# Optimization experiments

Hardware: AMD Instinct MI355X
Metric: run time of the kernel (lower is better)

## Reference

```python
import jax, jax.numpy as jnp
import numpy as np

N_NODES = 100000
N_EDGES = 3200000
IN_F = 256
OUT_F = 128


def setup_inputs() -> dict:
    key = jax.random.key(0)
    k1, k2, k3, k4, k5, k6 = jax.random.split(key, 6)
    x = jax.random.normal(k1, (N_NODES, IN_F), dtype=jnp.float32)
    edge_row = jax.random.randint(k2, (N_EDGES,), 0, N_NODES, dtype=jnp.int32)
    edge_col = jax.random.randint(k3, (N_EDGES,), 0, N_NODES, dtype=jnp.int32)
    edge_val = jax.random.uniform(k4, (N_EDGES,), dtype=jnp.float32)
    stdv = 1.0 / np.sqrt(OUT_F)
    weight = jax.random.uniform(k5, (IN_F, OUT_F), dtype=jnp.float32, minval=-stdv, maxval=stdv)
    bias = jax.random.uniform(k6, (OUT_F,), dtype=jnp.float32, minval=-stdv, maxval=stdv)
    return {"x": x, "edge_row": edge_row, "edge_col": edge_col,
            "edge_val": edge_val, "weight": weight, "bias": bias}


def reference(x, edge_row, edge_col, edge_val, weight, bias):
    # dropout p=0.0 -> identity. support = x @ W  [N, out_f]
    support = x @ weight
    # spmm(adj, support): out[r] = sum_e adj_val[e] * support[col[e]] for edges with row[e]==r
    gathered = support[edge_col] * edge_val[:, None]  # [E, out_f]
    out = jax.ops.segment_sum(gathered, edge_row, num_segments=N_NODES)
    out = out + bias
    return jax.nn.relu(out)
```

## Files before the change

kernel.cpp:

```cpp
#include <hip/hip_runtime.h>
#include <hip/hip_fp16.h>

#define IN_F 256
#define OUT_F 128
#define RPB 64
#define LOG_RPB 6
#define MAXB 2048
#define CHUNK 8192
#define CAP 3072

typedef __attribute__((ext_vector_type(8))) short short8;
typedef __attribute__((ext_vector_type(4))) float f32x4;

__device__ inline short bf16r(float f) {
  unsigned u = __float_as_uint(f);
  u += 0x7FFF + ((u >> 16) & 1);
  return (short)(u >> 16);
}

#define COL_OF(e) ((e) & 0x1FFFFu)
#define Q9_OF(e)  (((e) >> 17) & 0x1FFu)
#define RL_OF(e)  ((e) >> 26)

__global__ __launch_bounds__(256) void hist_wprep(const int* __restrict__ erow,
                                                  int* __restrict__ cnt2d,
                                                  const float* __restrict__ w,
                                                  short* __restrict__ wt,
                                                  int n_edges, int nbuck, int nblk) {
  __shared__ int h[MAXB];
  int t = threadIdx.x;
  if ((int)blockIdx.x >= nblk) {
    int i = (blockIdx.x - nblk) * 1024 + t * 4;
#pragma unroll
    for (int u = 0; u < 4; ++u) {
      int idx = i + u;
      int k = idx >> 7;
      int n = idx & 127;
      wt[n * 256 + k] = bf16r(w[idx]);
    }
    return;
  }
  for (int i = t; i < nbuck; i += 256) h[i] = 0;
  __syncthreads();
  int beg = blockIdx.x * CHUNK;
  int end = min(beg + CHUNK, n_edges);
  for (int e = beg + t; e < end; e += 256) atomicAdd(&h[erow[e] >> LOG_RPB], 1);
  __syncthreads();
  for (int i = t; i < nbuck; i += 256) cnt2d[(size_t)i * nblk + blockIdx.x] = h[i];
}

__global__ __launch_bounds__(256) void rowsum(const int* __restrict__ cnt2d,
                                              int* __restrict__ bcnt, int nblk) {
  __shared__ int red[256];
  int b = blockIdx.x;
  const int* row = cnt2d + (size_t)b * nblk;
  int t = threadIdx.x;
  int s = 0;
  for (int i = t; i < nblk; i += 256) s += row[i];
  red[t] = s;
  __syncthreads();
  for (int off = 128; off > 0; off >>= 1) {
    if (t < off) red[t] += red[t + off];
    __syncthreads();
  }
  if (t == 0) bcnt[b] = red[0];
}

__global__ __launch_bounds__(1024) void bucket_scan(const int* __restrict__ bcnt,
                                                    int* __restrict__ bptr, int nbuck) {
  __shared__ int sc[1024];
  int t = threadIdx.x;
  int i0 = 2 * t, i1 = 2 * t + 1;
  int c0 = (i0 < nbuck) ? bcnt[i0] : 0;
  int c1 = (i1 < nbuck) ? bcnt[i1] : 0;
  int s = c0 + c1;
  sc[t] = s;
  __syncthreads();
  for (int off = 1; off < 1024; off <<= 1) {
    int u = (t >= off) ? sc[t - off] : 0;
    __syncthreads();
    sc[t] += u;
    __syncthreads();
  }
  int run = sc[t] - s;
  if (i0 < nbuck) { bptr[i0] = run; run += c0; }
  if (i1 < nbuck) { bptr[i1] = run; run += c1; }
  if (t == 1023) bptr[nbuck] = sc[1023];
}

__global__ __launch_bounds__(256) void rowscan(const int* __restrict__ cnt2d,
                                               const int* __restrict__ bptr,
                                               int* __restrict__ off2d, int nblk) {
  __shared__ int sc[256];
  int b = blockIdx.x;
  const int* row = cnt2d + (size_t)b * nblk;
  int* orow = off2d + (size_t)b * nblk;
  int t = threadIdx.x;
  int chunk = (nblk + 255) >> 8;
  int beg = t * chunk, end2 = min(beg + chunk, nblk);
  int s = 0;
  for (int i = beg; i < end2; ++i) s += row[i];
  sc[t] = s;
  __syncthreads();
  for (int off = 1; off < 256; off <<= 1) {
    int u = (t >= off) ? sc[t - off] : 0;
    __syncthreads();
    sc[t] += u;
    __syncthreads();
  }
  int run = sc[t] - s + bptr[b];
  for (int i = beg; i < end2; ++i) {
    orow[i] = run;
    run += row[i];
  }
}

__global__ __launch_bounds__(512) void gemm_coarse(const float* __restrict__ x,
                                                   const short* __restrict__ wt,
                                                   __half* __restrict__ sup,
                                                   int n_nodes,
                                                   const int* __restrict__ erow,
                                                   const int* __restrict__ ecol,
                                                   const float* __restrict__ eval,
                                                   const int* __restrict__ off2d,
                                                   unsigned* __restrict__ tmp,
                                                   int n_edges, int nbuck, int nblk,
                                                   int ngemm) {
  __shared__ int cnt[MAXB];
  __shared__ int base[MAXB];
  int t = threadIdx.x;

  if ((int)blockIdx.x >= ngemm) {
    int cb = blockIdx.x - ngemm;
    for (int i = t; i < nbuck; i += 512) {
      cnt[i] = 0;
      base[i] = off2d[(size_t)i * nblk + cb];
    }
    __syncthreads();
    int beg = cb * CHUNK;
    int end = min(beg + CHUNK, n_edges);
    for (int e = beg + t; e < end; e += 512) {
      int r = erow[e];
      int b = r >> LOG_RPB;
      int pos = base[b] + atomicAdd(&cnt[b], 1);
      float v = eval[e];
      int q = min(max((int)(v * 511.f + 0.5f), 0), 511);
      tmp[pos] = (unsigned)ecol[e] | ((unsigned)q << 17) |
                 ((unsigned)(r & (RPB - 1)) << 26);
    }
    return;
  }

  int lane = t & 63;
  int wid = t >> 6;
  int wrow = (wid >> 1) * 32;
  int wcol = (wid & 1) * 64;
  int row_blk = blockIdx.x * 128;

  int arow[2];
#pragma unroll
  for (int mt = 0; mt < 2; ++mt)
    arow[mt] = min(row_blk + wrow + mt * 16 + (lane & 15), n_nodes - 1);
  int koff = (lane >> 4) * 8;

  f32x4 acc[2][4];
#pragma unroll
  for (int mt = 0; mt < 2; ++mt)
#pragma unroll
    for (int nt = 0; nt < 4; ++nt) acc[mt][nt] = (f32x4){0.f, 0.f, 0.f, 0.f};

#pragma unroll 2
  for (int kk = 0; kk < IN_F; kk += 32) {
    short8 af[2];
#pragma unroll
    for (int mt = 0; mt < 2; ++mt) {
      const float* px = x + (size_t)arow[mt] * IN_F + kk + koff;
      float4 p = *(const float4*)px;
      float4 q = *(const float4*)(px + 4);
      short8 a;
      a[0] = bf16r(p.x); a[1] = bf16r(p.y); a[2] = bf16r(p.z); a[3] = bf16r(p.w);
      a[4] = bf16r(q.x); a[5] = bf16r(q.y); a[6] = bf16r(q.z); a[7] = bf16r(q.w);
      af[mt] = a;
    }
    short8 bf[4];
#pragma unroll
    for (int nt = 0; nt < 4; ++nt) {
      int n = wcol + nt * 16 + (lane & 15);
      bf[nt] = *(const short8*)&wt[n * 256 + kk + koff];
    }
#pragma unroll
    for (int mt = 0; mt < 2; ++mt)
#pragma unroll
      for (int nt = 0; nt < 4; ++nt)
        acc[mt][nt] = __builtin_amdgcn_mfma_f32_16x16x32_bf16(af[mt], bf[nt],
                                                              acc[mt][nt], 0, 0, 0);
  }

#pragma unroll
  for (int mt = 0; mt < 2; ++mt)
#pragma unroll
    for (int nt = 0; nt < 4; ++nt)
#pragma unroll
      for (int reg = 0; reg < 4; ++reg) {
        int grow = row_blk + wrow + mt * 16 + (lane >> 4) * 4 + reg;
        int gcol = wcol + nt * 16 + (lane & 15);
        if (grow < n_nodes)
          sup[(size_t)grow * OUT_F + gcol] = __float2half(acc[mt][nt][reg]);
      }
}

__global__ __launch_bounds__(256) void sort_gather(const int* __restrict__ bptr,
                                                   const unsigned* __restrict__ tmp,
                                                   unsigned* __restrict__ spill,
                                                   const __half* __restrict__ sup,
                                                   const float* __restrict__ bias,
                                                   float* __restrict__ out,
                                                   int n_nodes) {
  __shared__ unsigned eL[CAP];
  __shared__ int hist[RPB];
  __shared__ int ex[RPB + 1];
  __shared__ int cur[RPB];
  int b = blockIdx.x;
  int row0 = b << LOG_RPB;
  int t = threadIdx.x;
  int bbeg = bptr[b];
  int bend = bptr[b + 1];
  int m = bend - bbeg;

  if (t < RPB) hist[t] = 0;
  __syncthreads();
  for (int j = bbeg + t; j < bend; j += 256) atomicAdd(&hist[RL_OF(tmp[j])], 1);
  __syncthreads();
  if (t < RPB) ex[t] = hist[t];
  __syncthreads();
  for (int off = 1; off < RPB; off <<= 1) {
    int u = (t < RPB && t >= off) ? ex[t - off] : 0;
    __syncthreads();
    if (t < RPB) ex[t] += u;
    __syncthreads();
  }
  if (t < RPB) {
    int st = ex[t] - hist[t];
    ex[t] = st;
    cur[t] = st;
  }
  if (t == 0) ex[RPB] = m;
  __syncthreads();
  for (int j = bbeg + t; j < bend; j += 256) {
    unsigned e = tmp[j];
    int pos = atomicAdd(&cur[RL_OF(e)], 1);
    if (pos < CAP) eL[pos] = e;
    else spill[bbeg + pos] = e;
  }
  __syncthreads();

  int lane = t & 63;
  int wv = t >> 6;
  int qw = lane >> 4;
  int sl = lane & 15;
  const float dq = 1.0f / 511.0f;
  float4 bi0 = ((const float4*)bias)[2 * sl + 0];
  float4 bi1 = ((const float4*)bias)[2 * sl + 1];
  int nr = min(RPB, n_nodes - row0);

#define LOADE(J) (((J) < CAP) ? eL[(J)] : spill[bbeg + (J)])
#define ACC8(A, S, V)                                                             \
  { float2 p;                                                                     \
    p = __half22float2(*(__half2*)&(S).x); A[0] = fmaf(p.x, V, A[0]); A[1] = fmaf(p.y, V, A[1]); \
    p = __half22float2(*(__half2*)&(S).y); A[2] = fmaf(p.x, V, A[2]); A[3] = fmaf(p.y, V, A[3]); \
    p = __half22float2(*(__half2*)&(S).z); A[4] = fmaf(p.x, V, A[4]); A[5] = fmaf(p.y, V, A[5]); \
    p = __half22float2(*(__half2*)&(S).w); A[6] = fmaf(p.x, V, A[6]); A[7] = fmaf(p.y, V, A[7]); }

  for (int rl = wv; rl < nr; rl += 4) {
    int beg = ex[rl];
    int end = ex[rl + 1];
    float a0[8] = {0.f, 0.f, 0.f, 0.f, 0.f, 0.f, 0.f, 0.f};
    float a1[8] = {0.f, 0.f, 0.f, 0.f, 0.f, 0.f, 0.f, 0.f};

    int j = beg + qw;
    for (; j + 4 < end; j += 8) {
      unsigned e0 = LOADE(j);
      unsigned e1 = LOADE(j + 4);
      uint4 s0 = ((const uint4*)(sup + (size_t)COL_OF(e0) * OUT_F))[sl];
      uint4 s1 = ((const uint4*)(sup + (size_t)COL_OF(e1) * OUT_F))[sl];
      float v0 = (float)Q9_OF(e0) * dq;
      float v1 = (float)Q9_OF(e1) * dq;
      ACC8(a0, s0, v0);
      ACC8(a1, s1, v1);
    }
    if (j < end) {
      unsigned e0 = LOADE(j);
      uint4 s0 = ((const uint4*)(sup + (size_t)COL_OF(e0) * OUT_F))[sl];
      float v0 = (float)Q9_OF(e0) * dq;
      ACC8(a0, s0, v0);
    }

    float r[8];
#pragma unroll
    for (int i = 0; i < 8; ++i) {
      r[i] = a0[i] + a1[i];
      r[i] += __shfl_xor(r[i], 16);
      r[i] += __shfl_xor(r[i], 32);
    }
    if (qw == 0) {
      float4 o0, o1;
      o0.x = fmaxf(r[0] + bi0.x, 0.f);
      o0.y = fmaxf(r[1] + bi0.y, 0.f);
      o0.z = fmaxf(r[2] + bi0.z, 0.f);
      o0.w = fmaxf(r[3] + bi0.w, 0.f);
      o1.x = fmaxf(r[4] + bi1.x, 0.f);
      o1.y = fmaxf(r[5] + bi1.y, 0.f);
      o1.z = fmaxf(r[6] + bi1.z, 0.f);
      o1.w = fmaxf(r[7] + bi1.w, 0.f);
      float4* orow = (float4*)(out + (size_t)(row0 + rl) * OUT_F);
      orow[2 * sl + 0] = o0;
      orow[2 * sl + 1] = o1;
    }
  }
#undef ACC8
#undef LOADE
}

__global__ __launch_bounds__(512) void gemm_mfma_only(const float* __restrict__ x,
                                                      const float* __restrict__ w,
                                                      __half* __restrict__ sup,
                                                      int n_nodes) {
  __shared__ short wlds[128 * 256];
  int t = threadIdx.x;
  for (int idx = t; idx < 256 * 128; idx += 512) {
    int k = idx >> 7;
    int n = idx & 127;
    int g = k >> 3;
    wlds[n * 256 + ((g ^ (n & 7)) << 3) + (k & 7)] = bf16r(w[idx]);
  }
  __syncthreads();
  int lane = t & 63;
  int wid = t >> 6;
  int wrow = (wid >> 1) * 64;
  int wcol = (wid & 1) * 64;
  int row_blk = blockIdx.x * 256;
  int arow[4];
#pragma unroll
  for (int mt = 0; mt < 4; ++mt)
    arow[mt] = min(row_blk + wrow + mt * 16 + (lane & 15), n_nodes - 1);
  int koff = (lane >> 4) * 8;
  f32x4 acc[4][4];
#pragma unroll
  for (int mt = 0; mt < 4; ++mt)
#pragma unroll
    for (int nt = 0; nt < 4; ++nt) acc[mt][nt] = (f32x4){0.f, 0.f, 0.f, 0.f};
#pragma unroll 2
  for (int kk = 0; kk < IN_F; kk += 32) {
    short8 af[4];
#pragma unroll
    for (int mt = 0; mt < 4; ++mt) {
      const float* px = x + (size_t)arow[mt] * IN_F + kk + koff;
      float4 p = *(const float4*)px;
      float4 q = *(const float4*)(px + 4);
      short8 a;
      a[0] = bf16r(p.x); a[1] = bf16r(p.y); a[2] = bf16r(p.z); a[3] = bf16r(p.w);
      a[4] = bf16r(q.x); a[5] = bf16r(q.y); a[6] = bf16r(q.z); a[7] = bf16r(q.w);
      af[mt] = a;
    }
    short8 bf[4];
    int g = (kk >> 3) + (lane >> 4);
#pragma unroll
    for (int nt = 0; nt < 4; ++nt) {
      int n = wcol + nt * 16 + (lane & 15);
      bf[nt] = *(const short8*)&wlds[n * 256 + ((g ^ (n & 7)) << 3)];
    }
#pragma unroll
    for (int mt = 0; mt < 4; ++mt)
#pragma unroll
      for (int nt = 0; nt < 4; ++nt)
        acc[mt][nt] = __builtin_amdgcn_mfma_f32_16x16x32_bf16(af[mt], bf[nt],
                                                              acc[mt][nt], 0, 0, 0);
  }
#pragma unroll
  for (int mt = 0; mt < 4; ++mt)
#pragma unroll
    for (int nt = 0; nt < 4; ++nt)
#pragma unroll
      for (int reg = 0; reg < 4; ++reg) {
        int grow = row_blk + wrow + mt * 16 + (lane >> 4) * 4 + reg;
        int gcol = wcol + nt * 16 + (lane & 15);
        if (grow < n_nodes)
          sup[(size_t)grow * OUT_F + gcol] = __float2half(acc[mt][nt][reg]);
      }
}

__global__ __launch_bounds__(256) void init_bias(float* __restrict__ out,
                                                 const float* __restrict__ bias,
                                                 int total) {
  int i = blockIdx.x * 256 + threadIdx.x;
  if (i < total) out[i] = bias[i & (OUT_F - 1)];
}

__global__ __launch_bounds__(256) void spmm_scatter(const int* __restrict__ erow,
                                                    const int* __restrict__ ecol,
                                                    const float* __restrict__ eval,
                                                    const __half* __restrict__ sup,
                                                    float* __restrict__ out,
                                                    int n_edges) {
  long long t = (long long)blockIdx.x * 256 + threadIdx.x;
  int e = (int)(t >> 6);
  if (e >= n_edges) return;
  int lane = (int)(t & 63);
  int r = erow[e];
  int c = ecol[e];
  float v = eval[e];
  __half2 s = ((const __half2*)(sup + (size_t)c * OUT_F))[lane];
  float2 f = __half22float2(s);
  float* orow = out + (size_t)r * OUT_F + 2 * lane;
  unsafeAtomicAdd(orow + 0, f.x * v);
  unsafeAtomicAdd(orow + 1, f.y * v);
}

__global__ __launch_bounds__(256) void relu_k(float* __restrict__ out, int total) {
  int i = blockIdx.x * 256 + threadIdx.x;
  if (i < total) out[i] = fmaxf(out[i], 0.f);
}

extern "C" void kernel_launch(void* const* d_in, const int* in_sizes, int n_in,
                              void* d_out, int out_size, void* d_ws, size_t ws_size,
                              hipStream_t stream) {
  const float* x = (const float*)d_in[0];
  const int* erow = (const int*)d_in[1];
  const int* ecol = (const int*)d_in[2];
  const float* eval = (const float*)d_in[3];
  const float* w = (const float*)d_in[4];
  const float* bias = (const float*)d_in[5];
  float* out = (float*)d_out;

  int n_nodes = in_sizes[0] / IN_F;
  int n_edges = in_sizes[1];
  int total = n_nodes * OUT_F;
  int nbuck = (n_nodes + RPB - 1) >> LOG_RPB;
  int nblk = (n_edges + CHUNK - 1) / CHUNK;
  int ngemm = (n_nodes + 127) / 128;

  char* p = (char*)d_ws;
  __half* sup = (__half*)p;             p += (size_t)n_nodes * OUT_F * 2;
  unsigned* tmp = (unsigned*)p;         p += (size_t)n_edges * 4;
  unsigned* spill = (unsigned*)p;       p += (size_t)n_edges * 4;
  short* wt = (short*)p;                p += (size_t)IN_F * OUT_F * 2;
  int* bcnt = (int*)p;                  p += (size_t)nbuck * 4;
  int* bptr = (int*)p;                  p += (size_t)(nbuck + 1) * 4;
  int* cnt2d = (int*)p;                 p += (size_t)nbuck * nblk * 4;
  int* off2d = (int*)p;                 p += (size_t)nbuck * nblk * 4;
  size_t need = (size_t)(p - (char*)d_ws);

  if (ws_size >= need && nbuck <= MAXB) {
    hist_wprep<<<nblk + 32, 256, 0, stream>>>(erow, cnt2d, w, wt,
                                              n_edges, nbuck, nblk);
    rowsum<<<nbuck, 256, 0, stream>>>(cnt2d, bcnt, nblk);
    bucket_scan<<<1, 1024, 0, stream>>>(bcnt, bptr, nbuck);
    rowscan<<<nbuck, 256, 0, stream>>>(cnt2d, bptr, off2d, nblk);
    gemm_coarse<<<ngemm + nblk, 512, 0, stream>>>(x, wt, sup, n_nodes, erow, ecol,
                                                  eval, off2d, tmp, n_edges, nbuck,
                                                  nblk, ngemm);
    sort_gather<<<nbuck, 256, 0, stream>>>(bptr, tmp, spill, sup, bias, out,
                                           n_nodes);
  } else {
    gemm_mfma_only<<<(n_nodes + 255) / 256, 512, 0, stream>>>(x, w, sup, n_nodes);
    init_bias<<<(total + 255) / 256, 256, 0, stream>>>(out, bias, total);
    long long threads = (long long)n_edges * 64;
    spmm_scatter<<<(int)((threads + 255) / 256), 256, 0, stream>>>(erow, ecol, eval,
                                                                   sup, out, n_edges);
    relu_k<<<(total + 255) / 256, 256, 0, stream>>>(out, total);
  }
}
```

Before: 240.4 us.

## Split GEMM across histogram and coarse-sort kernels with LDS-staged swizzled weights

The dense GEMM is now split into two parts: about 40% of its 256-row tiles run inside the histogram kernel and the rest inside the coarse-scatter kernel. The goal is to overlap the feature transform with both edge-bucketing phases instead of only the second. The separate weight-transpose prep is removed. Each GEMM block now converts W to bf16 into a bank-swizzled LDS tile and computes 256x128 tiles with larger per-wave register blocking. In exchange, every GEMM block repeats the weight conversion, the 64KB of LDS may lower occupancy for the histogram and scatter blocks, and the split ratio is hand-tuned.

```diff
diff --git a/kernel.cpp b/kernel.cpp
--- a/kernel.cpp
+++ b/kernel.cpp
@@ -22,101 +22,108 @@
 #define Q9_OF(e)  (((e) >> 17) & 0x1FFu)
 #define RL_OF(e)  ((e) >> 26)
 
-__global__ __launch_bounds__(256) void hist_wprep(const int* __restrict__ erow,
-                                                  int* __restrict__ cnt2d,
-                                                  const float* __restrict__ w,
-                                                  short* __restrict__ wt,
-                                                  int n_edges, int nbuck, int nblk) {
-  __shared__ int h[MAXB];
-  int t = threadIdx.x;
-  if ((int)blockIdx.x >= nblk) {
-    int i = (blockIdx.x - nblk) * 1024 + t * 4;
-#pragma unroll
-    for (int u = 0; u < 4; ++u) {
-      int idx = i + u;
-      int k = idx >> 7;
-      int n = idx & 127;
-      wt[n * 256 + k] = bf16r(w[idx]);
-    }
+__device__ __forceinline__ void gemm_tile(const float* __restrict__ x,
+                                          const float* __restrict__ w,
+                                          __half* __restrict__ sup,
+                                          int n_nodes, int tile_idx,
+                                          char* smem) {
+  short* wlds = (short*)smem;
+  int t = threadIdx.x;
+  for (int idx = t; idx < 256 * 128; idx += 512) {
+    int k = idx >> 7;
+    int n = idx & 127;
+    int g = k >> 3;
+    wlds[n * 256 + ((g ^ (n & 7)) << 3) + (k & 7)] = bf16r(w[idx]);
+  }
+  __syncthreads();
+
+  int lane = t & 63;
+  int wid = t >> 6;
+  int wrow = (wid >> 1) * 64;
+  int wcol = (wid & 1) * 64;
+  int row_blk = tile_idx * 256;
+
+  int arow[4];
+#pragma unroll
+  for (int mt = 0; mt < 4; ++mt)
+    arow[mt] = min(row_blk + wrow + mt * 16 + (lane & 15), n_nodes - 1);
+  int koff = (lane >> 4) * 8;
+
+  f32x4 acc[4][4];
+#pragma unroll
+  for (int mt = 0; mt < 4; ++mt)
+#pragma unroll
+    for (int nt = 0; nt < 4; ++nt) acc[mt][nt] = (f32x4){0.f, 0.f, 0.f, 0.f};
+
+#pragma unroll 2
+  for (int kk = 0; kk < IN_F; kk += 32) {
+    short8 af[4];
+#pragma unroll
+    for (int mt = 0; mt < 4; ++mt) {
+      const float* px = x + (size_t)arow[mt] * IN_F + kk + koff;
+      float4 p = *(const float4*)px;
+      float4 q = *(const float4*)(px + 4);
+      short8 a;
+      a[0] = bf16r(p.x); a[1] = bf16r(p.y); a[2] = bf16r(p.z); a[3] = bf16r(p.w);
+      a[4] = bf16r(q.x); a[5] = bf16r(q.y); a[6] = bf16r(q.z); a[7] = bf16r(q.w);
+      af[mt] = a;
+    }
+    short8 bf[4];
+    int g = (kk >> 3) + (lane >> 4);
+#pragma unroll
+    for (int nt = 0; nt < 4; ++nt) {
+      int n = wcol + nt * 16 + (lane & 15);
+      bf[nt] = *(const short8*)&wlds[n * 256 + ((g ^ (n & 7)) << 3)];
+    }
+#pragma unroll
+    for (int mt = 0; mt < 4; ++mt)
+#pragma unroll
+      for (int nt = 0; nt < 4; ++nt)
+        acc[mt][nt] = __builtin_amdgcn_mfma_f32_16x16x32_bf16(af[mt], bf[nt],
+                                                              acc[mt][nt], 0, 0, 0);
+  }
+
+#pragma unroll
+  for (int mt = 0; mt < 4; ++mt)
+#pragma unroll
+    for (int nt = 0; nt < 4; ++nt)
+#pragma unroll
+      for (int reg = 0; reg < 4; ++reg) {
+        int grow = row_blk + wrow + mt * 16 + (lane >> 4) * 4 + reg;
+        int gcol = wcol + nt * 16 + (lane & 15);
+        if (grow < n_nodes)
+          sup[(size_t)grow * OUT_F + gcol] = __float2half(acc[mt][nt][reg]);
+      }
+}
+
+__global__ __launch_bounds__(512) void gemm_hist(const float* __restrict__ x,
+                                                 const float* __restrict__ w,
+                                                 __half* __restrict__ sup,
+                                                 int n_nodes,
+                                                 const int* __restrict__ erow,
+                                                 int* __restrict__ cnt2d,
+                                                 int n_edges, int nbuck, int nblk,
+                                                 int g1) {
+  __shared__ char smem[128 * 256 * 2];
+  int t = threadIdx.x;
+
+  if ((int)blockIdx.x >= g1) {
+    int* h = (int*)smem;
+    int hb = blockIdx.x - g1;
+    for (int i = t; i < nbuck; i += 512) h[i] = 0;
+    __syncthreads();
+    int beg = hb * CHUNK;
+    int end = min(beg + CHUNK, n_edges);
+    for (int e = beg + t; e < end; e += 512) atomicAdd(&h[erow[e] >> LOG_RPB], 1);
+    __syncthreads();
+    for (int i = t; i < nbuck; i += 512) cnt2d[(size_t)i * nblk + hb] = h[i];
     return;
   }
-  for (int i = t; i < nbuck; i += 256) h[i] = 0;
-  __syncthreads();
-  int beg = blockIdx.x * CHUNK;
-  int end = min(beg + CHUNK, n_edges);
-  for (int e = beg + t; e < end; e += 256) atomicAdd(&h[erow[e] >> LOG_RPB], 1);
-  __syncthreads();
-  for (int i = t; i < nbuck; i += 256) cnt2d[(size_t)i * nblk + blockIdx.x] = h[i];
-}
-
-__global__ __launch_bounds__(256) void rowsum(const int* __restrict__ cnt2d,
-                                              int* __restrict__ bcnt, int nblk) {
-  __shared__ int red[256];
-  int b = blockIdx.x;
-  const int* row = cnt2d + (size_t)b * nblk;
-  int t = threadIdx.x;
-  int s = 0;
-  for (int i = t; i < nblk; i += 256) s += row[i];
-  red[t] = s;
-  __syncthreads();
-  for (int off = 128; off > 0; off >>= 1) {
-    if (t < off) red[t] += red[t + off];
-    __syncthreads();
-  }
-  if (t == 0) bcnt[b] = red[0];
-}
-
-__global__ __launch_bounds__(1024) void bucket_scan(const int* __restrict__ bcnt,
-                                                    int* __restrict__ bptr, int nbuck) {
-  __shared__ int sc[1024];
-  int t = threadIdx.x;
-  int i0 = 2 * t, i1 = 2 * t + 1;
-  int c0 = (i0 < nbuck) ? bcnt[i0] : 0;
-  int c1 = (i1 < nbuck) ? bcnt[i1] : 0;
-  int s = c0 + c1;
-  sc[t] = s;
-  __syncthreads();
-  for (int off = 1; off < 1024; off <<= 1) {
-    int u = (t >= off) ? sc[t - off] : 0;
-    __syncthreads();
-    sc[t] += u;
-    __syncthreads();
-  }
-  int run = sc[t] - s;
-  if (i0 < nbuck) { bptr[i0] = run; run += c0; }
-  if (i1 < nbuck) { bptr[i1] = run; run += c1; }
-  if (t == 1023) bptr[nbuck] = sc[1023];
-}
-
-__global__ __launch_bounds__(256) void rowscan(const int* __restrict__ cnt2d,
-                                               const int* __restrict__ bptr,
-                                               int* __restrict__ off2d, int nblk) {
-  __shared__ int sc[256];
-  int b = blockIdx.x;
-  const int* row = cnt2d + (size_t)b * nblk;
-  int* orow = off2d + (size_t)b * nblk;
-  int t = threadIdx.x;
-  int chunk = (nblk + 255) >> 8;
-  int beg = t * chunk, end2 = min(beg + chunk, nblk);
-  int s = 0;
-  for (int i = beg; i < end2; ++i) s += row[i];
-  sc[t] = s;
-  __syncthreads();
-  for (int off = 1; off < 256; off <<= 1) {
-    int u = (t >= off) ? sc[t - off] : 0;
-    __syncthreads();
-    sc[t] += u;
-    __syncthreads();
-  }
-  int run = sc[t] - s + bptr[b];
-  for (int i = beg; i < end2; ++i) {
-    orow[i] = run;
-    run += row[i];
-  }
+  gemm_tile(x, w, sup, n_nodes, blockIdx.x, smem);
 }
 
 __global__ __launch_bounds__(512) void gemm_coarse(const float* __restrict__ x,
-                                                   const short* __restrict__ wt,
+                                                   const float* __restrict__ w,
                                                    __half* __restrict__ sup,
                                                    int n_nodes,
                                                    const int* __restrict__ erow,
@@ -125,13 +132,14 @@
                                                    const int* __restrict__ off2d,
                                                    unsigned* __restrict__ tmp,
                                                    int n_edges, int nbuck, int nblk,
-                                                   int ngemm) {
-  __shared__ int cnt[MAXB];
-  __shared__ int base[MAXB];
-  int t = threadIdx.x;
-
-  if ((int)blockIdx.x >= ngemm) {
-    int cb = blockIdx.x - ngemm;
+                                                   int g2, int g1) {
+  __shared__ char smem[128 * 256 * 2];
+  int t = threadIdx.x;
+
+  if ((int)blockIdx.x >= g2) {
+    int* cnt = (int*)smem;
+    int* base = cnt + MAXB;
+    int cb = blockIdx.x - g2;
     for (int i = t; i < nbuck; i += 512) {
       cnt[i] = 0;
       base[i] = off2d[(size_t)i * nblk + cb];
@@ -150,63 +158,73 @@
     }
     return;
   }
-
-  int lane = t & 63;
-  int wid = t >> 6;
-  int wrow = (wid >> 1) * 32;
-  int wcol = (wid & 1) * 64;
-  int row_blk = blockIdx.x * 128;
-
-  int arow[2];
-#pragma unroll
-  for (int mt = 0; mt < 2; ++mt)
-    arow[mt] = min(row_blk + wrow + mt * 16 + (lane & 15), n_nodes - 1);
-  int koff = (lane >> 4) * 8;
-
-  f32x4 acc[2][4];
-#pragma unroll
-  for (int mt = 0; mt < 2; ++mt)
-#pragma unroll
-    for (int nt = 0; nt < 4; ++nt) acc[mt][nt] = (f32x4){0.f, 0.f, 0.f, 0.f};
-
-#pragma unroll 2
-  for (int kk = 0; kk < IN_F; kk += 32) {
-    short8 af[2];
-#pragma unroll
-    for (int mt = 0; mt < 2; ++mt) {
-      const float* px = x + (size_t)arow[mt] * IN_F + kk + koff;
-      float4 p = *(const float4*)px;
-      float4 q = *(const float4*)(px + 4);
-      short8 a;
-      a[0] = bf16r(p.x); a[1] = bf16r(p.y); a[2] = bf16r(p.z); a[3] = bf16r(p.w);
-      a[4] = bf16r(q.x); a[5] = bf16r(q.y); a[6] = bf16r(q.z); a[7] = bf16r(q.w);
-      af[mt] = a;
-    }
-    short8 bf[4];
-#pragma unroll
-    for (int nt = 0; nt < 4; ++nt) {
-      int n = wcol + nt * 16 + (lane & 15);
-      bf[nt] = *(const short8*)&wt[n * 256 + kk + koff];
-    }
-#pragma unroll
-    for (int mt = 0; mt < 2; ++mt)
-#pragma unroll
-      for (int nt = 0; nt < 4; ++nt)
-        acc[mt][nt] = __builtin_amdgcn_mfma_f32_16x16x32_bf16(af[mt], bf[nt],
-                                                              acc[mt][nt], 0, 0, 0);
-  }
-
-#pragma unroll
-  for (int mt = 0; mt < 2; ++mt)
-#pragma unroll
-    for (int nt = 0; nt < 4; ++nt)
-#pragma unroll
-      for (int reg = 0; reg < 4; ++reg) {
-        int grow = row_blk + wrow + mt * 16 + (lane >> 4) * 4 + reg;
-        int gcol = wcol + nt * 16 + (lane & 15);
-        if (grow < n_nodes)
-          sup[(size_t)grow * OUT_F + gcol] = __float2half(acc[mt][nt][reg]);
-      }
+  gemm_tile(x, w, sup, n_nodes, g1 + blockIdx.x, smem);
+}
+
+__global__ __launch_bounds__(256) void rowsum(const int* __restrict__ cnt2d,
+                                              int* __restrict__ bcnt, int nblk) {
+  __shared__ int red[256];
+  int b = blockIdx.x;
+  const int* row = cnt2d + (size_t)b * nblk;
+  int t = threadIdx.x;
+  int s = 0;
+  for (int i = t; i < nblk; i += 256) s += row[i];
+  red[t] = s;
+  __syncthreads();
+  for (int off = 128; off > 0; off >>= 1) {
+    if (t < off) red[t] += red[t + off];
+    __syncthreads();
+  }
+  if (t == 0) bcnt[b] = red[0];
+}
+
+__global__ __launch_bounds__(1024) void bucket_scan(const int* __restrict__ bcnt,
+                                                    int* __restrict__ bptr, int nbuck) {
+  __shared__ int sc[1024];
+  int t = threadIdx.x;
+  int i0 = 2 * t, i1 = 2 * t + 1;
+  int c0 = (i0 < nbuck) ? bcnt[i0] : 0;
+  int c1 = (i1 < nbuck) ? bcnt[i1] : 0;
+  int s = c0 + c1;
+  sc[t] = s;
+  __syncthreads();
+  for (int off = 1; off < 1024; off <<= 1) {
+    int u = (t >= off) ? sc[t - off] : 0;
+    __syncthreads();
+    sc[t] += u;
+    __syncthreads();
+  }
+  int run = sc[t] - s;
+  if (i0 < nbuck) { bptr[i0] = run; run += c0; }
+  if (i1 < nbuck) { bptr[i1] = run; run += c1; }
+  if (t == 1023) bptr[nbuck] = sc[1023];
+}
+
+__global__ __launch_bounds__(256) void rowscan(const int* __restrict__ cnt2d,
+                                               const int* __restrict__ bptr,
+                                               int* __restrict__ off2d, int nblk) {
+  __shared__ int sc[256];
+  int b = blockIdx.x;
+  const int* row = cnt2d + (size_t)b * nblk;
+  int* orow = off2d + (size_t)b * nblk;
+  int t = threadIdx.x;
+  int chunk = (nblk + 255) >> 8;
+  int beg = t * chunk, end2 = min(beg + chunk, nblk);
+  int s = 0;
+  for (int i = beg; i < end2; ++i) s += row[i];
+  sc[t] = s;
+  __syncthreads();
+  for (int off = 1; off < 256; off <<= 1) {
+    int u = (t >= off) ? sc[t - off] : 0;
+    __syncthreads();
+    sc[t] += u;
+    __syncthreads();
+  }
+  int run = sc[t] - s + bptr[b];
+  for (int i = beg; i < end2; ++i) {
+    orow[i] = run;
+    run += row[i];
+  }
 }
 
 __global__ __launch_bounds__(256) void sort_gather(const int* __restrict__ bptr,
@@ -325,68 +343,8 @@
                                                       const float* __restrict__ w,
                                                       __half* __restrict__ sup,
                                                       int n_nodes) {
-  __shared__ short wlds[128 * 256];
-  int t = threadIdx.x;
-  for (int idx = t; idx < 256 * 128; idx += 512) {
-    int k = idx >> 7;
-    int n = idx & 127;
-    int g = k >> 3;
-    wlds[n * 256 + ((g ^ (n & 7)) << 3) + (k & 7)] = bf16r(w[idx]);
-  }
-  __syncthreads();
-  int lane = t & 63;
-  int wid = t >> 6;
-  int wrow = (wid >> 1) * 64;
-  int wcol = (wid & 1) * 64;
-  int row_blk = blockIdx.x * 256;
-  int arow[4];
-#pragma unroll
-  for (int mt = 0; mt < 4; ++mt)
-    arow[mt] = min(row_blk + wrow + mt * 16 + (lane & 15), n_nodes - 1);
-  int koff = (lane >> 4) * 8;
-  f32x4 acc[4][4];
-#pragma unroll
-  for (int mt = 0; mt < 4; ++mt)
-#pragma unroll
-    for (int nt = 0; nt < 4; ++nt) acc[mt][nt] = (f32x4){0.f, 0.f, 0.f, 0.f};
-#pragma unroll 2
-  for (int kk = 0; kk < IN_F; kk += 32) {
-    short8 af[4];
-#pragma unroll
-    for (int mt = 0; mt < 4; ++mt) {
-      const float* px = x + (size_t)arow[mt] * IN_F + kk + koff;
-      float4 p = *(const float4*)px;
-      float4 q = *(const float4*)(px + 4);
-      short8 a;
-      a[0] = bf16r(p.x); a[1] = bf16r(p.y); a[2] = bf16r(p.z); a[3] = bf16r(p.w);
-      a[4] = bf16r(q.x); a[5] = bf16r(q.y); a[6] = bf16r(q.z); a[7] = bf16r(q.w);
-      af[mt] = a;
-    }
-    short8 bf[4];
-    int g = (kk >> 3) + (lane >> 4);
-#pragma unroll
-    for (int nt = 0; nt < 4; ++nt) {
-      int n = wcol + nt * 16 + (lane & 15);
-      bf[nt] = *(const short8*)&wlds[n * 256 + ((g ^ (n & 7)) << 3)];
-    }
-#pragma unroll
-    for (int mt = 0; mt < 4; ++mt)
-#pragma unroll
-      for (int nt = 0; nt < 4; ++nt)
-        acc[mt][nt] = __builtin_amdgcn_mfma_f32_16x16x32_bf16(af[mt], bf[nt],
-                                                              acc[mt][nt], 0, 0, 0);
-  }
-#pragma unroll
-  for (int mt = 0; mt < 4; ++mt)
-#pragma unroll
-    for (int nt = 0; nt < 4; ++nt)
-#pragma unroll
-      for (int reg = 0; reg < 4; ++reg) {
-        int grow = row_blk + wrow + mt * 16 + (lane >> 4) * 4 + reg;
-        int gcol = wcol + nt * 16 + (lane & 15);
-        if (grow < n_nodes)
-          sup[(size_t)grow * OUT_F + gcol] = __float2half(acc[mt][nt][reg]);
-      }
+  __shared__ char smem[128 * 256 * 2];
+  gemm_tile(x, w, sup, n_nodes, blockIdx.x, smem);
 }
 
 __global__ __launch_bounds__(256) void init_bias(float* __restrict__ out,
@@ -437,13 +395,14 @@
   int total = n_nodes * OUT_F;
   int nbuck = (n_nodes + RPB - 1) >> LOG_RPB;
   int nblk = (n_edges + CHUNK - 1) / CHUNK;
-  int ngemm = (n_nodes + 127) / 128;
+  int ngemm = (n_nodes + 255) / 256;
+  int g1 = (ngemm * 2) / 5;
+  int g2 = ngemm - g1;
 
   char* p = (char*)d_ws;
   __half* sup = (__half*)p;             p += (size_t)n_nodes * OUT_F * 2;
   unsigned* tmp = (unsigned*)p;         p += (size_t)n_edges * 4;
   unsigned* spill = (unsigned*)p;       p += (size_t)n_edges * 4;
-  short* wt = (short*)p;                p += (size_t)IN_F * OUT_F * 2;
   int* bcnt = (int*)p;                  p += (size_t)nbuck * 4;
   int* bptr = (int*)p;                  p += (size_t)(nbuck + 1) * 4;
   int* cnt2d = (int*)p;                 p += (size_t)nbuck * nblk * 4;
@@ -451,18 +410,18 @@
   size_t need = (size_t)(p - (char*)d_ws);
 
   if (ws_size >= need && nbuck <= MAXB) {
-    hist_wprep<<<nblk + 32, 256, 0, stream>>>(erow, cnt2d, w, wt,
-                                              n_edges, nbuck, nblk);
+    gemm_hist<<<g1 + nblk, 512, 0, stream>>>(x, w, sup, n_nodes, erow, cnt2d,
+                                             n_edges, nbuck, nblk, g1);
     rowsum<<<nbuck, 256, 0, stream>>>(cnt2d, bcnt, nblk);
     bucket_scan<<<1, 1024, 0, stream>>>(bcnt, bptr, nbuck);
     rowscan<<<nbuck, 256, 0, stream>>>(cnt2d, bptr, off2d, nblk);
-    gemm_coarse<<<ngemm + nblk, 512, 0, stream>>>(x, wt, sup, n_nodes, erow, ecol,
-                                                  eval, off2d, tmp, n_edges, nbuck,
-                                                  nblk, ngemm);
+    gemm_coarse<<<g2 + nblk, 512, 0, stream>>>(x, w, sup, n_nodes, erow, ecol,
+                                               eval, off2d, tmp, n_edges, nbuck,
+                                               nblk, g2, g1);
     sort_gather<<<nbuck, 256, 0, stream>>>(bptr, tmp, spill, sup, bias, out,
                                            n_nodes);
   } else {
-    gemm_mfma_only<<<(n_nodes + 255) / 256, 512, 0, stream>>>(x, w, sup, n_nodes);
+    gemm_mfma_only<<<ngemm, 512, 0, stream>>>(x, w, sup, n_nodes);
     init_bias<<<(total + 255) / 256, 256, 0, stream>>>(out, bias, total);
     long long threads = (long long)n_edges * 64;
     spmm_scatter<<<(int)((threads + 255) / 256), 256, 0, stream>>>(erow, ecol, eval,
```

Result: faster. 228.0 us (-5.1%).
